# Performance work log

Measured on AMD Instinct MI355X. Metric: run time of the kernel, lower is better.

The kernel has to match this reference:

```python
import jax, jax.numpy as jnp
import numpy as np
import math

N_HEADS = 16
D_EMBED = 1024
D_CROSS = 768
FF_DIM = 4096
D_HEAD = D_EMBED // N_HEADS
LN_EPS = 1e-5


def layer_norm(h, g, b):
    mu = jnp.mean(h, axis=-1, keepdims=True)
    var = jnp.var(h, axis=-1, keepdims=True)
    return (h - mu) * jax.lax.rsqrt(var + LN_EPS) * g + b


def mha(q, k, v):
    # q: [B,Sq,D], k/v: [B,Skv,D] -> split heads, attend, merge
    B, Sq, _ = q.shape
    Skv = k.shape[1]
    qh = q.reshape(B, Sq, N_HEADS, D_HEAD).transpose(0, 2, 1, 3)
    kh = k.reshape(B, Skv, N_HEADS, D_HEAD).transpose(0, 2, 1, 3)
    vh = v.reshape(B, Skv, N_HEADS, D_HEAD).transpose(0, 2, 1, 3)
    scores = jnp.einsum('bhqd,bhkd->bhqk', qh, kh) / math.sqrt(D_HEAD)
    attn = jax.nn.softmax(scores, axis=-1)
    out = jnp.einsum('bhqk,bhkd->bhqd', attn, vh)
    return out.transpose(0, 2, 1, 3).reshape(B, Sq, D_EMBED)


def setup_inputs() -> dict:
    key = jax.random.key(0)
    ks = jax.random.split(key, 24)
    s = 0.02
    inp = {
        'x': jax.random.normal(ks[0], (4, 1024, D_EMBED), jnp.float32),
        'y': jax.random.normal(ks[1], (4, 77, D_CROSS), jnp.float32),
        # self-attention in_proj (d_embed -> 3*d_embed) and out_proj
        'w_qkv': jax.random.normal(ks[2], (D_EMBED, 3 * D_EMBED), jnp.float32) * s,
        'b_qkv': jnp.zeros((3 * D_EMBED,), jnp.float32),
        'w_so': jax.random.normal(ks[3], (D_EMBED, D_EMBED), jnp.float32) * s,
        'b_so': jnp.zeros((D_EMBED,), jnp.float32),
        # cross-attention projections
        'w_q': jax.random.normal(ks[4], (D_EMBED, D_EMBED), jnp.float32) * s,
        'b_q': jnp.zeros((D_EMBED,), jnp.float32),
        'w_k': jax.random.normal(ks[5], (D_CROSS, D_EMBED), jnp.float32) * s,
        'b_k': jnp.zeros((D_EMBED,), jnp.float32),
        'w_v': jax.random.normal(ks[6], (D_CROSS, D_EMBED), jnp.float32) * s,
        'b_v': jnp.zeros((D_EMBED,), jnp.float32),
        'w_co': jax.random.normal(ks[7], (D_EMBED, D_EMBED), jnp.float32) * s,
        'b_co': jnp.zeros((D_EMBED,), jnp.float32),
        # 3-layer FFN
        'w1': jax.random.normal(ks[8], (D_EMBED, FF_DIM), jnp.float32) * s,
        'b1': jnp.zeros((FF_DIM,), jnp.float32),
        'w2': jax.random.normal(ks[9], (FF_DIM, FF_DIM), jnp.float32) * s,
        'b2': jnp.zeros((FF_DIM,), jnp.float32),
        'w3': jax.random.normal(ks[10], (FF_DIM, D_EMBED), jnp.float32) * s,
        'b3': jnp.zeros((D_EMBED,), jnp.float32),
        # single shared LayerNorm (used 3 times, as in the torch module)
        'ln_g': jnp.ones((D_EMBED,), jnp.float32),
        'ln_b': jnp.zeros((D_EMBED,), jnp.float32),
    }
    return inp


def reference(x, y, w_qkv, b_qkv, w_so, b_so, w_q, b_q, w_k, b_k, w_v, b_v,
              w_co, b_co, w1, b1, w2, b2, w3, b3, ln_g, ln_b):
    # --- self attention (no causal mask) ---
    qkv = x @ w_qkv + b_qkv
    q, k, v = jnp.split(qkv, 3, axis=-1)
    sa = mha(q, k, v) @ w_so + b_so
    x = layer_norm(x + sa, ln_g, ln_b)
    # --- cross attention ---
    qc = x @ w_q + b_q
    kc = y @ w_k + b_k
    vc = y @ w_v + b_v
    ca = mha(qc, kc, vc) @ w_co + b_co
    x = layer_norm(x + ca, ln_g, ln_b)
    # --- 3-layer FFN with ReLU ---
    h = jax.nn.relu(x @ w1 + b1)
    h = jax.nn.relu(h @ w2 + b2)
    ff = h @ w3 + b3
    x = layer_norm(x + ff, ln_g, ln_b)
    return x
```

## Files before the change

### kernel.cpp

```cpp
#include <hip/hip_runtime.h>
#include <hip/hip_bf16.h>
#include <math.h>

typedef short v8s __attribute__((ext_vector_type(8)));
typedef short v4s __attribute__((ext_vector_type(4)));
typedef float v4f __attribute__((ext_vector_type(4)));

__device__ __forceinline__ unsigned short f2bf(float f) {
  union { float f; unsigned u; } a; a.f = f;
  unsigned u = a.u + 0x7fffu + ((a.u >> 16) & 1u);
  return (unsigned short)(u >> 16);
}

__device__ __forceinline__ void gld_lds16(const unsigned short* g, unsigned short* l) {
  __builtin_amdgcn_global_load_lds(
      (const __attribute__((address_space(1))) void*)g,
      (__attribute__((address_space(3))) void*)l,
      16, 0, 0);
}

#define VMCNT(n)  asm volatile("s_waitcnt vmcnt(" #n ")" ::: "memory")
#define LGKM(n)   asm volatile("s_waitcnt lgkmcnt(" #n ")" ::: "memory")

__global__ void cvt_f32_bf16(const float* __restrict__ in,
                             unsigned short* __restrict__ out, int n4) {
  int i = blockIdx.x * blockDim.x + threadIdx.x;
  if (i >= n4) return;
  float4 v = reinterpret_cast<const float4*>(in)[i];
  ushort4 o;
  o.x = f2bf(v.x); o.y = f2bf(v.y); o.z = f2bf(v.z); o.w = f2bf(v.w);
  reinterpret_cast<ushort4*>(out)[i] = o;
}

__global__ void cvt_transpose(const float* __restrict__ in,
                              unsigned short* __restrict__ out, int K, int N) {
  __shared__ float t[32][33];
  int bx = blockIdx.x, by = blockIdx.y;
  int tx = threadIdx.x, ty = threadIdx.y;
#pragma unroll
  for (int i = 0; i < 4; i++) {
    int k = by * 32 + ty + i * 8;
    t[ty + i * 8][tx] = in[(size_t)k * N + bx * 32 + tx];
  }
  __syncthreads();
#pragma unroll
  for (int i = 0; i < 4; i++) {
    int n = bx * 32 + ty + i * 8;
    out[(size_t)n * K + by * 32 + tx] = f2bf(t[tx][ty + i * 8]);
  }
}

__global__ __launch_bounds__(256)
void transpose_v(const unsigned short* __restrict__ V,
                 unsigned short* __restrict__ Vt,
                 int rowstride, int batch_rows, int Skv, int kvpad) {
  __shared__ __align__(16) unsigned short t[64][80];
  int ch = blockIdx.x, h = blockIdx.y, b = blockIdx.z;
  int tid = threadIdx.x;
  int sr = tid >> 2, sc = (tid & 3) * 16;
  int gr = ch * 64 + sr;
  v8s v0 = {}, v1 = {};
  if (gr < Skv) {
    const unsigned short* p = V + (size_t)(b * batch_rows + gr) * rowstride + h * 64 + sc;
    v0 = *(const v8s*)p; v1 = *(const v8s*)(p + 8);
  }
  *(v8s*)&t[sr][sc]     = v0;
  *(v8s*)&t[sr][sc + 8] = v1;
  __syncthreads();
  int d  = tid >> 2;
  int k0 = (tid & 3) * 16;
  unsigned short* o = Vt + ((size_t)(b * 16 + h) * 64 + d) * kvpad + ch * 64 + k0;
  v8s o0, o1;
#pragma unroll
  for (int e = 0; e < 8; e++) { o0[e] = t[k0 + e][d]; o1[e] = t[k0 + 8 + e][d]; }
  *(v8s*)o       = o0;
  *(v8s*)(o + 8) = o1;
}

#define PH_MFMA(AFR, IB, JB)                                                   \
  _Pragma("unroll")                                                            \
  for (int m = 0; m < 4; m++) {                                                \
    _Pragma("unroll")                                                          \
    for (int n = 0; n < 2; n++) {                                              \
      acc[IB + m][JB + n] = __builtin_amdgcn_mfma_f32_16x16x32_bf16(           \
          AFR[m][0], bF[n][0], acc[IB + m][JB + n], 0, 0, 0);                  \
      acc[IB + m][JB + n] = __builtin_amdgcn_mfma_f32_16x16x32_bf16(           \
          AFR[m][1], bF[n][1], acc[IB + m][JB + n], 0, 0, 0);                  \
    }                                                                          \
  }

template<bool RELU>
__global__ __launch_bounds__(512, 2)
void gemm256(const unsigned short* __restrict__ A,
             const unsigned short* __restrict__ BT,
             const float* __restrict__ bias,
             unsigned short* __restrict__ Cb,
             int M, int N, int K, int lda, int ldb) {
  __shared__ __align__(16) unsigned short lA[2][2][8192];
  __shared__ __align__(16) unsigned short lB[2][2][8192];
  int tid  = threadIdx.x;
  int lane = tid & 63;
  int wave = tid >> 6;
  int wrow = wave >> 2;
  int wcol = wave & 3;
  int quad = lane >> 4;
  int l15  = lane & 15;
  int m0 = blockIdx.y * 256;
  int n0 = blockIdx.x * 256;
  int NT = K >> 6;

  int lrow = lane >> 3;
  int swz8 = ((lane & 7) ^ lrow) << 3;
  const unsigned short* gA0 = A + (size_t)(m0 + wave * 8 + lrow) * lda + swz8;
  int rr = wave * 8 + lrow;
  int nbase = (rr >> 5) * 64 + (rr & 31);
  const unsigned short* gB0 = BT + (size_t)(n0 + nbase) * ldb + swz8;

  auto stageA = [&](int U, int h, int rlo) {
    unsigned short* d = &lA[U & 1][h][(rlo + wave * 8) * 64];
    gld_lds16(gA0 + (size_t)(h * 128 + rlo) * lda + (size_t)U * 64, d);
  };
  auto stageB = [&](int U, int hB, int q) {
    unsigned short* d = &lB[U & 1][hB][(q * 64 + wave * 8) * 64];
    gld_lds16(gB0 + (size_t)(q * 128 + hB * 32) * ldb + (size_t)U * 64, d);
  };

  int ch0 = (quad ^ (l15 & 7)) << 3;
  int ch1 = ch0 ^ 32;
  int wcol32 = wcol * 32;

  const v4f vzero = {0.f, 0.f, 0.f, 0.f};
  v4f acc[8][4];
#pragma unroll
  for (int i = 0; i < 8; i++)
#pragma unroll
    for (int j = 0; j < 4; j++) acc[i][j] = vzero;

  v8s aF0[4][2], aF1[4][2], bF[2][2];

  stageA(0, 0, 0);  stageA(0, 1, 0);
  stageB(0, 0, 0);  stageB(0, 0, 1);
  stageA(0, 0, 64); stageA(0, 1, 64);
  stageB(0, 1, 0);  stageB(0, 1, 1);
  if (NT > 1) {
    stageA(1, 0, 0);  stageA(1, 1, 0);
    stageB(1, 0, 0);  stageB(1, 0, 1);
    stageA(1, 0, 64); stageA(1, 1, 64);
    VMCNT(8);
  } else {
    VMCNT(0);
  }
  __builtin_amdgcn_s_barrier();

  for (int U = 0; U < NT; ++U) {
    int c = U & 1;
    bool tail = (U + 3 >= NT);
    const unsigned short* pA  = &lA[c][wrow][0];
    const unsigned short* pB0 = &lB[c][0][0];
    const unsigned short* pB1 = &lB[c][1][0];

#pragma unroll
    for (int m = 0; m < 4; m++) {
      int ro = (m * 16 + l15) * 64;
      aF0[m][0] = *(const v8s*)&pA[ro + ch0];
      aF0[m][1] = *(const v8s*)&pA[ro + ch1];
    }
#pragma unroll
    for (int n = 0; n < 2; n++) {
      int ro = (wcol32 + n * 16 + l15) * 64;
      bF[n][0] = *(const v8s*)&pB0[ro + ch0];
      bF[n][1] = *(const v8s*)&pB0[ro + ch1];
    }
    if (U + 1 < NT) { stageB(U + 1, 1, 0); stageB(U + 1, 1, 1); }
    LGKM(8);
    __builtin_amdgcn_s_barrier();
    LGKM(0);
    __builtin_amdgcn_sched_barrier(0);
    __builtin_amdgcn_s_setprio(1);
    PH_MFMA(aF0, 0, 0)
    __builtin_amdgcn_s_setprio(0);
    __builtin_amdgcn_s_barrier();

#pragma unroll
    for (int m = 0; m < 4; m++) {
      int ro = (64 * 64) + (m * 16 + l15) * 64;
      aF1[m][0] = *(const v8s*)&pA[ro + ch0];
      aF1[m][1] = *(const v8s*)&pA[ro + ch1];
    }
    if (U + 2 < NT) { stageA(U + 2, 0, 0); stageA(U + 2, 1, 0); }
    __builtin_amdgcn_s_barrier();
    LGKM(0);
    __builtin_amdgcn_sched_barrier(0);
    __builtin_amdgcn_s_setprio(1);
    PH_MFMA(aF1, 4, 0)
    __builtin_amdgcn_s_setprio(0);
    if (tail) { VMCNT(0); } else { VMCNT(10); }
    __builtin_amdgcn_s_barrier();

#pragma unroll
    for (int n = 0; n < 2; n++) {
      int ro = (wcol32 + n * 16 + l15) * 64;
      bF[n][0] = *(const v8s*)&pB1[ro + ch0];
      bF[n][1] = *(const v8s*)&pB1[ro + ch1];
    }
    if (U + 2 < NT) { stageB(U + 2, 0, 0); stageB(U + 2, 0, 1); }
    __builtin_amdgcn_s_barrier();
    LGKM(0);
    __builtin_amdgcn_sched_barrier(0);
    __builtin_amdgcn_s_setprio(1);
    PH_MFMA(aF1, 4, 2)
    __builtin_amdgcn_s_setprio(0);
    __builtin_amdgcn_s_barrier();

    if (U + 2 < NT) { stageA(U + 2, 0, 64); stageA(U + 2, 1, 64); }
    __builtin_amdgcn_s_barrier();
    __builtin_amdgcn_s_setprio(1);
    PH_MFMA(aF0, 0, 2)
    __builtin_amdgcn_s_setprio(0);
    if (tail) { VMCNT(0); } else { VMCNT(8); }
    __builtin_amdgcn_s_barrier();
  }

#pragma unroll
  for (int j = 0; j < 4; j++) {
    int col = n0 + wcol * 64 + (j >> 1) * 32 + (j & 1) * 16 + l15;
    float bv = bias[col];
#pragma unroll
    for (int i = 0; i < 8; i++) {
      int rb = m0 + wrow * 128 + (i >> 2) * 64 + (i & 3) * 16 + quad * 4;
#pragma unroll
      for (int r = 0; r < 4; r++) {
        int row = rb + r;
        if (row < M) {
          float v = acc[i][j][r] + bv;
          if (RELU) v = fmaxf(v, 0.f);
          Cb[(size_t)row * N + col] = f2bf(v);
        }
      }
    }
  }
}

template<bool RELU, bool OUTF, bool OUTB>
__global__ __launch_bounds__(256)
void gemm_bf16(const unsigned short* __restrict__ A,
               const unsigned short* __restrict__ BT,
               const float* __restrict__ bias,
               const float* __restrict__ bias2, int bsplit,
               float* __restrict__ Cf, float* __restrict__ Cf2,
               unsigned short* __restrict__ Cb,
               int M, int N, int Kred, int ld) {
  __shared__ __align__(16) unsigned short lA[128 * 64];
  __shared__ __align__(16) unsigned short lB[128 * 64];
  int tid  = threadIdx.x;
  int lane = tid & 63;
  int wave = tid >> 6;
  int wr = (wave >> 1) * 64;
  int wc = (wave & 1) * 64;
  int quad = lane >> 4;
  int l15  = lane & 15;
  int m0 = blockIdx.y * 128;
  int n0 = blockIdx.x * 128;
  int z  = blockIdx.z;

  const unsigned short* Az = A  + (size_t)z * Kred;
  const unsigned short* Bz = BT + (size_t)z * Kred;
  float* Cfo = z ? Cf2 : Cf;
  const float* biasz = z ? nullptr : bias;

  int srow   = tid >> 3;
  int schunk = (tid & 7) ^ (srow & 7);
  const unsigned short* gA = Az + (size_t)(m0 + srow) * ld + schunk * 8;
  const unsigned short* gB = Bz + (size_t)(n0 + srow) * ld + schunk * 8;
  unsigned short* ldsA = lA + wave * 512;
  unsigned short* ldsB = lB + wave * 512;
  const size_t rowblk = (size_t)32 * ld;

  const v4f vzero = {0.f, 0.f, 0.f, 0.f};
  v4f acc[4][4];
#pragma unroll
  for (int i = 0; i < 4; i++)
#pragma unroll
    for (int j = 0; j < 4; j++) acc[i][j] = vzero;

  for (int k0 = 0; k0 < Kred; k0 += 64) {
#pragma unroll
    for (int i = 0; i < 4; i++) {
      gld_lds16(gA + k0 + i * rowblk, ldsA + i * 2048);
      gld_lds16(gB + k0 + i * rowblk, ldsB + i * 2048);
    }
    __syncthreads();
#pragma unroll
    for (int s = 0; s < 2; s++) {
      v8s aF[4], bF[4];
#pragma unroll
      for (int i = 0; i < 4; i++)
        aF[i] = *(const v8s*)&lA[(wr + i * 16 + l15) * 64 + (((s * 4 + quad) ^ (l15 & 7)) * 8)];
#pragma unroll
      for (int j = 0; j < 4; j++)
        bF[j] = *(const v8s*)&lB[(wc + j * 16 + l15) * 64 + (((s * 4 + quad) ^ (l15 & 7)) * 8)];
#pragma unroll
      for (int i = 0; i < 4; i++)
#pragma unroll
        for (int j = 0; j < 4; j++)
          acc[i][j] = __builtin_amdgcn_mfma_f32_16x16x32_bf16(aF[i], bF[j], acc[i][j], 0, 0, 0);
    }
    __syncthreads();
  }

#pragma unroll
  for (int j = 0; j < 4; j++) {
    int col = n0 + wc + j * 16 + l15;
    float bv = 0.f;
    if (biasz) bv = (bias2 && col >= bsplit) ? bias2[col - bsplit] : biasz[col];
#pragma unroll
    for (int i = 0; i < 4; i++) {
#pragma unroll
      for (int r = 0; r < 4; r++) {
        int row = m0 + wr + i * 16 + quad * 4 + r;
        if (row < M) {
          float v = acc[i][j][r] + bv;
          if (RELU) v = fmaxf(v, 0.f);
          if (OUTF) Cfo[(size_t)row * N + col] = v;
          if (OUTB && !z) Cb[(size_t)row * N + col] = f2bf(v);
        }
      }
    }
  }
}

__global__ __launch_bounds__(256)
void attn_kernel(const unsigned short* __restrict__ Q,
                 const unsigned short* __restrict__ K,
                 const unsigned short* __restrict__ Vt,
                 unsigned short* __restrict__ O,
                 int q_rowstride, int kv_rowstride, int o_rowstride,
                 int q_batch_rows, int kv_batch_rows, int Skv, int kvpad,
                 float scale) {
  __shared__ __align__(16) unsigned short lK[64][72];
  __shared__ __align__(16) unsigned short lV[64][72];
  __shared__ __align__(16) unsigned short lP[4][16][72];
  int tid  = threadIdx.x;
  int lane = tid & 63;
  int wave = tid >> 6;
  int quad = lane >> 4;
  int l15  = lane & 15;
  int qt = blockIdx.x, h = blockIdx.y, b = blockIdx.z;

  const unsigned short* Qb  = Q  + (size_t)b * q_batch_rows * q_rowstride + h * 64;
  const unsigned short* Kb  = K  + (size_t)b * kv_batch_rows * kv_rowstride + h * 64;
  const unsigned short* Vtb = Vt + ((size_t)(b * 16 + h) * 64) * kvpad;

  v8s qf0, qf1;
  {
    const unsigned short* qr = Qb + (size_t)(qt * 64 + wave * 16 + l15) * q_rowstride + quad * 8;
    qf0 = *(const v8s*)(qr);
    qf1 = *(const v8s*)(qr + 32);
  }

  const v4f vzero = {0.f, 0.f, 0.f, 0.f};
  v4f o_acc[4];
#pragma unroll
  for (int t = 0; t < 4; t++) o_acc[t] = vzero;
  float m_r[4], l_r[4];
#pragma unroll
  for (int r = 0; r < 4; r++) { m_r[r] = -1e30f; l_r[r] = 0.f; }

  int sr = tid >> 2;
  int sc = (tid & 3) * 16;
  int nch = (Skv + 63) >> 6;

  v8s kv0 = {}, kv1 = {}, vv0, vv1;
  if (sr < Skv) {
    const unsigned short* kp = Kb + (size_t)sr * kv_rowstride + sc;
    kv0 = *(const v8s*)kp;  kv1 = *(const v8s*)(kp + 8);
  }
  {
    const unsigned short* vp = Vtb + (size_t)sr * kvpad + sc;
    vv0 = *(const v8s*)vp;  vv1 = *(const v8s*)(vp + 8);
  }

  for (int ch = 0; ch < nch; ch++) {
    int base = ch * 64;
    __builtin_amdgcn_s_barrier();
    __builtin_amdgcn_sched_barrier(0);
    *(v8s*)&lK[sr][sc]     = kv0;
    *(v8s*)&lK[sr][sc + 8] = kv1;
    {
      v4s a0 = {vv0[0], vv0[1], vv0[2], vv0[3]};
      v4s a1 = {vv0[4], vv0[5], vv0[6], vv0[7]};
      v4s a2 = {vv1[0], vv1[1], vv1[2], vv1[3]};
      v4s a3 = {vv1[4], vv1[5], vv1[6], vv1[7]};
      *(v4s*)&lV[sr][sc]      = a0;
      *(v4s*)&lV[sr][sc + 4]  = a1;
      *(v4s*)&lV[sr][sc + 8]  = a2;
      *(v4s*)&lV[sr][sc + 12] = a3;
    }
    v8s kn0 = {}, kn1 = {}, vn0 = {}, vn1 = {};
    if (ch + 1 < nch) {
      int gr2 = base + 64 + sr;
      if (gr2 < Skv) {
        const unsigned short* kp2 = Kb + (size_t)gr2 * kv_rowstride + sc;
        kn0 = *(const v8s*)kp2;  kn1 = *(const v8s*)(kp2 + 8);
      }
      const unsigned short* vp2 = Vtb + (size_t)sr * kvpad + base + 64 + sc;
      vn0 = *(const v8s*)vp2;  vn1 = *(const v8s*)(vp2 + 8);
    }
    LGKM(0);
    __builtin_amdgcn_s_barrier();
    __builtin_amdgcn_sched_barrier(0);

    float s[4][4];
#pragma unroll
    for (int t = 0; t < 4; t++) {
      v8s kf0 = *(const v8s*)&lK[t * 16 + l15][quad * 8];
      v8s kf1 = *(const v8s*)&lK[t * 16 + l15][32 + quad * 8];
      v4f sacc = vzero;
      sacc = __builtin_amdgcn_mfma_f32_16x16x32_bf16(qf0, kf0, sacc, 0, 0, 0);
      sacc = __builtin_amdgcn_mfma_f32_16x16x32_bf16(qf1, kf1, sacc, 0, 0, 0);
      int kvpos = base + t * 16 + l15;
      bool ok = kvpos < Skv;
#pragma unroll
      for (int r = 0; r < 4; r++) s[t][r] = ok ? sacc[r] * scale : -1e30f;
    }

#pragma unroll
    for (int r = 0; r < 4; r++) {
      float mx = fmaxf(fmaxf(s[0][r], s[1][r]), fmaxf(s[2][r], s[3][r]));
#pragma unroll
      for (int d = 1; d < 16; d <<= 1) mx = fmaxf(mx, __shfl_xor(mx, d));
      float mnew = fmaxf(m_r[r], mx);
      float alpha = __expf(m_r[r] - mnew);
      float sm = 0.f;
#pragma unroll
      for (int t = 0; t < 4; t++) { s[t][r] = __expf(s[t][r] - mnew); sm += s[t][r]; }
#pragma unroll
      for (int d = 1; d < 16; d <<= 1) sm += __shfl_xor(sm, d);
      l_r[r] = l_r[r] * alpha + sm;
      m_r[r] = mnew;
#pragma unroll
      for (int t = 0; t < 4; t++) o_acc[t][r] *= alpha;
    }

#pragma unroll
    for (int t = 0; t < 4; t++)
#pragma unroll
      for (int r = 0; r < 4; r++)
        lP[wave][quad * 4 + r][t * 16 + l15] = f2bf(s[t][r]);
    v8s pf0 = *(const v8s*)&lP[wave][l15][quad * 8];
    v8s pf1 = *(const v8s*)&lP[wave][l15][32 + quad * 8];
#pragma unroll
    for (int t = 0; t < 4; t++) {
      v8s vf0 = *(const v8s*)&lV[t * 16 + l15][quad * 8];
      v8s vf1 = *(const v8s*)&lV[t * 16 + l15][32 + quad * 8];
      o_acc[t] = __builtin_amdgcn_mfma_f32_16x16x32_bf16(pf0, vf0, o_acc[t], 0, 0, 0);
      o_acc[t] = __builtin_amdgcn_mfma_f32_16x16x32_bf16(pf1, vf1, o_acc[t], 0, 0, 0);
    }

    kv0 = kn0; kv1 = kn1; vv0 = vn0; vv1 = vn1;
  }

  int orow0 = b * q_batch_rows + qt * 64 + wave * 16;
#pragma unroll
  for (int t = 0; t < 4; t++) {
#pragma unroll
    for (int r = 0; r < 4; r++) {
      float v = o_acc[t][r] / l_r[r];
      O[(size_t)(orow0 + quad * 4 + r) * o_rowstride + h * 64 + t * 16 + l15] = f2bf(v);
    }
  }
}

__global__ __launch_bounds__(256)
void ln_kernel(const float* base, const float* __restrict__ delta,
               const float* __restrict__ delta2,
               const float* __restrict__ g, const float* __restrict__ bb,
               float* outf, unsigned short* __restrict__ outb) {
  __shared__ float red[8];
  int row = blockIdx.x;
  int tid = threadIdx.x;
  float4 vb = ((const float4*)(base  + (size_t)row * 1024))[tid];
  float4 vd = ((const float4*)(delta + (size_t)row * 1024))[tid];
  float v0 = vb.x + vd.x, v1 = vb.y + vd.y, v2 = vb.z + vd.z, v3 = vb.w + vd.w;
  if (delta2) {
    float4 v2d = ((const float4*)(delta2 + (size_t)row * 1024))[tid];
    v0 += v2d.x; v1 += v2d.y; v2 += v2d.z; v3 += v2d.w;
  }
  float s = v0 + v1 + v2 + v3;
  float q = v0 * v0 + v1 * v1 + v2 * v2 + v3 * v3;
#pragma unroll
  for (int d = 1; d < 64; d <<= 1) { s += __shfl_xor(s, d); q += __shfl_xor(q, d); }
  int wave = tid >> 6, lane = tid & 63;
  if (lane == 0) { red[wave] = s; red[4 + wave] = q; }
  __syncthreads();
  s = red[0] + red[1] + red[2] + red[3];
  q = red[4] + red[5] + red[6] + red[7];
  float mean = s * (1.f / 1024.f);
  float var  = q * (1.f / 1024.f) - mean * mean;
  float rstd = rsqrtf(var + 1e-5f);
  float4 gg  = ((const float4*)g)[tid];
  float4 bv  = ((const float4*)bb)[tid];
  float o0 = (v0 - mean) * rstd * gg.x + bv.x;
  float o1 = (v1 - mean) * rstd * gg.y + bv.y;
  float o2 = (v2 - mean) * rstd * gg.z + bv.z;
  float o3 = (v3 - mean) * rstd * gg.w + bv.w;
  if (outf) {
    float4 o; o.x = o0; o.y = o1; o.z = o2; o.w = o3;
    ((float4*)(outf + (size_t)row * 1024))[tid] = o;
  }
  if (outb) {
    ushort4 u; u.x = f2bf(o0); u.y = f2bf(o1); u.z = f2bf(o2); u.w = f2bf(o3);
    ((ushort4*)(outb + (size_t)row * 1024))[tid] = u;
  }
}

extern "C" void kernel_launch(void* const* d_in, const int* in_sizes, int n_in,
                              void* d_out, int out_size, void* d_ws, size_t ws_size,
                              hipStream_t stream) {
  const float* x     = (const float*)d_in[0];
  const float* y     = (const float*)d_in[1];
  const float* w_qkv = (const float*)d_in[2];
  const float* b_qkv = (const float*)d_in[3];
  const float* w_so  = (const float*)d_in[4];
  const float* b_so  = (const float*)d_in[5];
  const float* w_q   = (const float*)d_in[6];
  const float* b_q   = (const float*)d_in[7];
  const float* w_k   = (const float*)d_in[8];
  const float* b_k   = (const float*)d_in[9];
  const float* w_v   = (const float*)d_in[10];
  const float* b_v   = (const float*)d_in[11];
  const float* w_co  = (const float*)d_in[12];
  const float* b_co  = (const float*)d_in[13];
  const float* w1    = (const float*)d_in[14];
  const float* b1    = (const float*)d_in[15];
  const float* w2    = (const float*)d_in[16];
  const float* b2    = (const float*)d_in[17];
  const float* w3    = (const float*)d_in[18];
  const float* b3    = (const float*)d_in[19];
  const float* ln_g  = (const float*)d_in[20];
  const float* ln_b  = (const float*)d_in[21];

  char* ws = (char*)d_ws;
  auto US = [&](size_t off) { return (unsigned short*)(ws + off); };
  auto FP = [&](size_t off) { return (float*)(ws + off); };

  constexpr size_t o_wqkv = 0;
  constexpr size_t o_wso  = o_wqkv + 3072ull * 1024 * 2;
  constexpr size_t o_wq   = o_wso  + 1024ull * 1024 * 2;
  constexpr size_t o_wk   = o_wq   + 1024ull * 1024 * 2;
  constexpr size_t o_wv   = o_wk   + 1024ull * 768 * 2;
  constexpr size_t o_wco  = o_wv   + 1024ull * 768 * 2;
  constexpr size_t o_w1   = o_wco  + 1024ull * 1024 * 2;
  constexpr size_t o_w2   = o_w1   + 4096ull * 1024 * 2;
  constexpr size_t o_w3   = o_w2   + 4096ull * 4096 * 2;
  constexpr size_t o_xf   = o_w3   + 1024ull * 4096 * 2;
  constexpr size_t o_xbf  = o_xf   + 4096ull * 1024 * 4;
  constexpr size_t o_ybf  = o_xbf  + 4096ull * 1024 * 2;
  constexpr size_t o_dlt  = o_ybf  + 308ull * 768 * 2;
  constexpr size_t o_R1   = o_dlt  + 4096ull * 1024 * 4;
  constexpr size_t o_attn = o_R1   + 4096ull * 3072 * 2;
  constexpr size_t o_R2   = o_attn + 4096ull * 1024 * 2;
  constexpr size_t o_qc  = o_R1;
  constexpr size_t o_kc  = o_R1 + 4096ull * 1024 * 2;
  constexpr size_t o_h1  = o_R1;
  constexpr size_t o_h2  = o_R2;
  constexpr size_t o_dlt2 = o_R1;
  constexpr size_t o_vtS = o_R2;
  constexpr size_t o_vtC = o_R2 + 4ull * 16 * 64 * 1024 * 2;

  dim3 tb(32, 8);
  cvt_transpose<<<dim3(96, 32),  tb, 0, stream>>>(w_qkv, US(o_wqkv), 1024, 3072);
  cvt_transpose<<<dim3(32, 32),  tb, 0, stream>>>(w_so,  US(o_wso),  1024, 1024);
  cvt_transpose<<<dim3(32, 32),  tb, 0, stream>>>(w_q,   US(o_wq),   1024, 1024);
  cvt_transpose<<<dim3(32, 24),  tb, 0, stream>>>(w_k,   US(o_wk),   768,  1024);
  cvt_transpose<<<dim3(32, 24),  tb, 0, stream>>>(w_v,   US(o_wv),   768,  1024);
  cvt_transpose<<<dim3(32, 32),  tb, 0, stream>>>(w_co,  US(o_wco),  1024, 1024);
  cvt_transpose<<<dim3(128, 32), tb, 0, stream>>>(w1,    US(o_w1),   1024, 4096);
  cvt_transpose<<<dim3(128, 128),tb, 0, stream>>>(w2,    US(o_w2),   4096, 4096);
  cvt_transpose<<<dim3(32, 128), tb, 0, stream>>>(w3,    US(o_w3),   4096, 1024);

  cvt_f32_bf16<<<4096, 256, 0, stream>>>(x, US(o_xbf), 4096 * 1024 / 4);
  cvt_f32_bf16<<<231, 256, 0, stream>>>(y, US(o_ybf), 4 * 77 * 768 / 4);

  gemm256<false><<<dim3(12, 16), 512, 0, stream>>>(
      US(o_xbf), US(o_wqkv), b_qkv, US(o_R1), 4096, 3072, 1024, 1024, 1024);
  transpose_v<<<dim3(16, 16, 4), 256, 0, stream>>>(
      US(o_R1) + 2048, US(o_vtS), 3072, 1024, 1024, 1024);
  attn_kernel<<<dim3(16, 16, 4), 256, 0, stream>>>(
      US(o_R1), US(o_R1) + 1024, US(o_vtS), US(o_attn),
      3072, 3072, 1024, 1024, 1024, 1024, 1024, 0.125f);
  gemm_bf16<false, true, false><<<dim3(8, 32, 2), 256, 0, stream>>>(
      US(o_attn), US(o_wso), b_so, nullptr, 0,
      FP(o_dlt), FP(o_dlt2), nullptr, 4096, 1024, 512, 1024);
  ln_kernel<<<4096, 256, 0, stream>>>(x, FP(o_dlt), FP(o_dlt2), ln_g, ln_b,
                                      FP(o_xf), US(o_xbf));

  gemm_bf16<false, false, true><<<dim3(8, 32, 1), 256, 0, stream>>>(
      US(o_xbf), US(o_wq), b_q, nullptr, 0,
      nullptr, nullptr, US(o_qc), 4096, 1024, 1024, 1024);
  gemm_bf16<false, false, true><<<dim3(16, 3, 1), 256, 0, stream>>>(
      US(o_ybf), US(o_wk), b_k, b_v, 1024,
      nullptr, nullptr, US(o_kc), 308, 2048, 768, 768);
  transpose_v<<<dim3(2, 16, 4), 256, 0, stream>>>(
      US(o_kc) + 1024, US(o_vtC), 2048, 77, 77, 128);
  attn_kernel<<<dim3(16, 16, 4), 256, 0, stream>>>(
      US(o_qc), US(o_kc), US(o_vtC), US(o_attn),
      1024, 2048, 1024, 1024, 77, 77, 128, 0.125f);
  gemm_bf16<false, true, false><<<dim3(8, 32, 2), 256, 0, stream>>>(
      US(o_attn), US(o_wco), b_co, nullptr, 0,
      FP(o_dlt), FP(o_dlt2), nullptr, 4096, 1024, 512, 1024);
  ln_kernel<<<4096, 256, 0, stream>>>(FP(o_xf), FP(o_dlt), FP(o_dlt2), ln_g, ln_b,
                                      FP(o_xf), US(o_xbf));

  gemm256<true><<<dim3(16, 16), 512, 0, stream>>>(
      US(o_xbf), US(o_w1), b1, US(o_h1), 4096, 4096, 1024, 1024, 1024);
  gemm256<true><<<dim3(16, 16), 512, 0, stream>>>(
      US(o_h1), US(o_w2), b2, US(o_h2), 4096, 4096, 4096, 4096, 4096);
  gemm_bf16<false, true, false><<<dim3(8, 32, 2), 256, 0, stream>>>(
      US(o_h2), US(o_w3), b3, nullptr, 0,
      FP(o_dlt), FP(o_dlt2), nullptr, 4096, 1024, 2048, 4096);
  ln_kernel<<<4096, 256, 0, stream>>>(FP(o_xf), FP(o_dlt), FP(o_dlt2), ln_g, ln_b,
                                      (float*)d_out, nullptr);
}
```

Measured before the change: 735.9 us.

## Swizzle GEMM workgroup order, add lazy softmax rescale and MFMA priority hints

The GEMM kernel remaps flat workgroup IDs so that consecutive blocks are spread in strides of eight, intended to improve L2/MALL locality across XCDs. The attention kernel now rescales the running max, sum and output only when some row's new max exceeds the old one by more than 8. This skips the per-chunk exp and multiply work at the risk of larger intermediate values. It also wraps the MFMA sections in s_setprio raises to favour matrix-issue waves. The swizzle assumes the workgroup count is divisible by eight, otherwise the mapping can skip or duplicate tiles.

```diff
diff --git a/kernel.cpp b/kernel.cpp
--- a/kernel.cpp
+++ b/kernel.cpp
@@ -105,8 +105,13 @@
   int wcol = wave & 3;
   int quad = lane >> 4;
   int l15  = lane & 15;
-  int m0 = blockIdx.y * 256;
-  int n0 = blockIdx.x * 256;
+
+  int nwg  = gridDim.x * gridDim.y;
+  int flat = blockIdx.y * gridDim.x + blockIdx.x;
+  int q8   = nwg >> 3;
+  int swz  = (flat & 7) * q8 + (flat >> 3);
+  int m0 = (swz / gridDim.x) * 256;
+  int n0 = (swz % gridDim.x) * 256;
   int NT = K >> 6;
 
   int lrow = lane >> 3;
@@ -411,6 +416,7 @@
     __builtin_amdgcn_sched_barrier(0);
 
     float s[4][4];
+    __builtin_amdgcn_s_setprio(1);
 #pragma unroll
     for (int t = 0; t < 4; t++) {
       v8s kf0 = *(const v8s*)&lK[t * 16 + l15][quad * 8];
@@ -423,23 +429,38 @@
 #pragma unroll
       for (int r = 0; r < 4; r++) s[t][r] = ok ? sacc[r] * scale : -1e30f;
     }
-
+    __builtin_amdgcn_s_setprio(0);
+
+    float mxv[4];
 #pragma unroll
     for (int r = 0; r < 4; r++) {
       float mx = fmaxf(fmaxf(s[0][r], s[1][r]), fmaxf(s[2][r], s[3][r]));
 #pragma unroll
       for (int d = 1; d < 16; d <<= 1) mx = fmaxf(mx, __shfl_xor(mx, d));
-      float mnew = fmaxf(m_r[r], mx);
-      float alpha = __expf(m_r[r] - mnew);
+      mxv[r] = mx;
+    }
+    bool need = false;
+#pragma unroll
+    for (int r = 0; r < 4; r++) need = need || (mxv[r] > m_r[r] + 8.f);
+    if (__any(need)) {
+#pragma unroll
+      for (int r = 0; r < 4; r++) {
+        float mnew = fmaxf(m_r[r], mxv[r]);
+        float alpha = __expf(m_r[r] - mnew);
+        l_r[r] *= alpha;
+        m_r[r] = mnew;
+#pragma unroll
+        for (int t = 0; t < 4; t++) o_acc[t][r] *= alpha;
+      }
+    }
+#pragma unroll
+    for (int r = 0; r < 4; r++) {
       float sm = 0.f;
 #pragma unroll
-      for (int t = 0; t < 4; t++) { s[t][r] = __expf(s[t][r] - mnew); sm += s[t][r]; }
+      for (int t = 0; t < 4; t++) { s[t][r] = __expf(s[t][r] - m_r[r]); sm += s[t][r]; }
 #pragma unroll
       for (int d = 1; d < 16; d <<= 1) sm += __shfl_xor(sm, d);
-      l_r[r] = l_r[r] * alpha + sm;
-      m_r[r] = mnew;
-#pragma unroll
-      for (int t = 0; t < 4; t++) o_acc[t][r] *= alpha;
+      l_r[r] += sm;
     }
 
 #pragma unroll
@@ -449,6 +470,7 @@
         lP[wave][quad * 4 + r][t * 16 + l15] = f2bf(s[t][r]);
     v8s pf0 = *(const v8s*)&lP[wave][l15][quad * 8];
     v8s pf1 = *(const v8s*)&lP[wave][l15][32 + quad * 8];
+    __builtin_amdgcn_s_setprio(1);
 #pragma unroll
     for (int t = 0; t < 4; t++) {
       v8s vf0 = *(const v8s*)&lV[t * 16 + l15][quad * 8];
@@ -456,6 +478,7 @@
       o_acc[t] = __builtin_amdgcn_mfma_f32_16x16x32_bf16(pf0, vf0, o_acc[t], 0, 0, 0);
       o_acc[t] = __builtin_amdgcn_mfma_f32_16x16x32_bf16(pf1, vf1, o_acc[t], 0, 0, 0);
     }
+    __builtin_amdgcn_s_setprio(0);
 
     kv0 = kn0; kv1 = kn1; vv0 = vn0; vv1 = vn1;
   }
```

Result: no change. 742.4 us (+0.9%).
